# Optimization experiments

Measured on AMD Instinct MI355X. Metric: run time of the kernel, lower is better.

## Reference

```python
import jax, jax.numpy as jnp
import numpy as np

WINDOW = 512
GLOBAL = 64
NEG = -1e9


def setup_inputs() -> dict:
    key = jax.random.key(0)
    kq, kk, kv = jax.random.split(key, 3)
    B, H, S, D = 2, 16, 4096, 64
    q = jax.random.normal(kq, (B, H, S, D), dtype=jnp.float32)
    k = jax.random.normal(kk, (B, H, S, D), dtype=jnp.float32)
    v = jax.random.normal(kv, (B, H, S, D), dtype=jnp.float32)
    return {"q": q, "k": k, "v": v}


def _swa(q, k, v):
    # Causal sliding-window attention (window WINDOW, inclusive of self)
    # with the first GLOBAL queries attending to ALL keys (non-causal),
    # matching the torch reference's per-position SDPA loop.
    B, H, S, D = q.shape
    W, G = WINDOW, GLOBAL
    nb = S // W  # seq chosen as multiple of window
    scale = jnp.asarray(1.0 / np.sqrt(D), q.dtype)

    # --- banded (sliding-window) part, computed blockwise ---
    qb = q.reshape(B, H, nb, W, D)
    # pad one window of zeros in front so each query block sees blocks [b-1, b]
    kp = jnp.pad(k, ((0, 0), (0, 0), (W, 0), (0, 0))).reshape(B, H, nb + 1, W, D)
    vp = jnp.pad(v, ((0, 0), (0, 0), (W, 0), (0, 0))).reshape(B, H, nb + 1, W, D)
    kc = jnp.concatenate([kp[:, :, :nb], kp[:, :, 1:]], axis=3)  # (B,H,nb,2W,D)
    vc = jnp.concatenate([vp[:, :, :nb], vp[:, :, 1:]], axis=3)  # (B,H,nb,2W,D)

    scores = jnp.einsum("bhnqd,bhnkd->bhnqk", qb, kc) * scale  # (B,H,nb,W,2W)

    # query global pos i = b*W + r; key global pos j = (b-1)*W + c, c in [0,2W)
    # window constraint i-W+1 <= j <= i  <=>  r+1 <= c <= r+W
    r = jnp.arange(W)[:, None]
    c = jnp.arange(2 * W)[None, :]
    band = (c >= r + 1) & (c <= r + W)              # (W, 2W)
    first = band & (c >= W)                          # block 0: j >= 0
    blk0 = (jnp.arange(nb) == 0)[:, None, None]
    mask = jnp.where(blk0, first[None], band[None])  # (nb, W, 2W)

    scores = jnp.where(mask[None, None], scores, jnp.asarray(NEG, scores.dtype))
    probs = jax.nn.softmax(scores, axis=-1)
    out = jnp.einsum("bhnqk,bhnkd->bhnqd", probs, vc).reshape(B, H, S, D)

    # --- global prefix: first G queries attend to all keys ---
    sg = jnp.einsum("bhqd,bhkd->bhqk", q[:, :, :G], k) * scale  # (B,H,G,S)
    og = jnp.einsum("bhqk,bhkd->bhqd", jax.nn.softmax(sg, axis=-1), v)
    return out.at[:, :, :G].set(og)


def reference(q, k, v):
    return _swa(q, k, v)
```

## Files before the change

kernel.cpp:

```cpp
#include <hip/hip_runtime.h>


typedef __attribute__((ext_vector_type(4))) float  f32x4;
typedef __attribute__((ext_vector_type(8))) short  s16x8;

#define S_LEN  4096
#define D_HEAD 64
#define SCALE_L2 (0.125f * 1.44269504088896340736f)
#define MINIT  (-1e5f)
#define MASKV  (-1e30f)

static __device__ __forceinline__ short f2bf(float x) {
  unsigned u = __builtin_bit_cast(unsigned, x);
  return (short)((u + 0x8000u) >> 16);
}

static __device__ __forceinline__ f32x4 mfma32(s16x8 a, s16x8 b, f32x4 c) {
  return __builtin_amdgcn_mfma_f32_16x16x32_bf16(a, b, c, 0, 0, 0);
}

struct Stage {
  f32x4 ka[2][2];
  float vs[2][8];
};

static __device__ __forceinline__ void stage_load(const float* __restrict__ K,
                                                  const float* __restrict__ V,
                                                  int k0, int tid, Stage& st) {
#pragma unroll
  for (int i = 0; i < 2; ++i) {
    int s = tid + i * 256;
    int fb = s >> 6, ln = s & 63;
    {
      int row = k0 + ((fb >> 1) << 4) + (ln & 15);
      int d0  = ((fb & 1) << 5) + ((ln >> 4) << 3);
      const float* p = K + row * 64 + d0;
      st.ka[i][0] = *(const f32x4*)p;
      st.ka[i][1] = *(const f32x4*)(p + 4);
    }
    {
      int t = fb >> 2, dt = fb & 3;
      int dd = dt * 16 + (ln & 15);
      int kk = k0 + t * 32 + ((ln >> 4) << 2);
      const float* p = V + kk * 64 + dd;
#pragma unroll
      for (int j = 0; j < 4; ++j) { st.vs[i][j] = p[j * 64]; st.vs[i][4 + j] = p[(16 + j) * 64]; }
    }
  }
}

static __device__ __forceinline__ void stage_write(short* kf, short* vf, int tid, const Stage& st) {
#pragma unroll
  for (int i = 0; i < 2; ++i) {
    int s = tid + i * 256;
    s16x8 kr, vr;
#pragma unroll
    for (int e = 0; e < 4; ++e) { kr[e] = f2bf(st.ka[i][0][e]); kr[4 + e] = f2bf(st.ka[i][1][e]); }
#pragma unroll
    for (int e = 0; e < 8; ++e) vr[e] = f2bf(st.vs[i][e]);
    *(s16x8*)(kf + s * 8) = kr;
    *(s16x8*)(vf + s * 8) = vr;
  }
}

extern "C" __global__ void __launch_bounds__(256, 2)
swa_fused_kernel(const float* __restrict__ qg, const float* __restrict__ kg,
                 const float* __restrict__ vg, float* __restrict__ outg) {
  __shared__ __align__(16) short KB[2][4096];
  __shared__ __align__(16) short VB[2][4096];

  const int tid = threadIdx.x;
  const int w  = tid >> 6;
  const int l  = tid & 63;
  const int g  = l >> 4;
  const int ql = l & 15;
  const int bx = blockIdx.x;
  const int t  = bx >> 5;
  const int bh = bx & 31;

  const float* Q = qg + (size_t)bh * S_LEN * D_HEAD;
  const float* K = kg + (size_t)bh * S_LEN * D_HEAD;
  const float* V = vg + (size_t)bh * S_LEN * D_HEAD;
  float* O = outg + (size_t)bh * S_LEN * D_HEAD;

  Stage st;

  if (t == 0) {
    const int qrow = w * 16 + ql;
    s16x8 qf[2];
#pragma unroll
    for (int h = 0; h < 2; ++h) {
      const float* p = Q + qrow * 64 + h * 32 + g * 8;
      f32x4 a = *(const f32x4*)p, b = *(const f32x4*)(p + 4);
      s16x8 r;
#pragma unroll
      for (int e = 0; e < 4; ++e) { r[e] = f2bf(a[e] * SCALE_L2); r[4 + e] = f2bf(b[e] * SCALE_L2); }
      qf[h] = r;
    }
    f32x4 acc[4] = {{0,0,0,0},{0,0,0,0},{0,0,0,0},{0,0,0,0}};
    float m = MINIT, lsum = 0.f;

    stage_load(K, V, 0, tid, st);
    stage_write(KB[0], VB[0], tid, st);
    __syncthreads();
    int cur = 0;
    for (int kb = 0; kb < 64; ++kb) {
      if (kb < 63) stage_load(K, V, (kb + 1) * 64, tid, st);
      const short* kf = KB[cur];
      const short* vf = VB[cur];
      f32x4 c[4];
#pragma unroll
      for (int kt = 0; kt < 4; ++kt) {
        s16x8 a0 = *(const s16x8*)(kf + ((kt * 2 + 0) * 64 + l) * 8);
        s16x8 a1 = *(const s16x8*)(kf + ((kt * 2 + 1) * 64 + l) * 8);
        f32x4 z = {0,0,0,0};
        z = mfma32(a0, qf[0], z);
        c[kt] = mfma32(a1, qf[1], z);
      }
      float rm = MASKV;
#pragma unroll
      for (int kt = 0; kt < 4; ++kt)
#pragma unroll
        for (int r = 0; r < 4; ++r) rm = fmaxf(rm, c[kt][r]);
      rm = fmaxf(rm, __shfl_xor(rm, 16));
      rm = fmaxf(rm, __shfl_xor(rm, 32));
      float mn = fmaxf(m, rm);
      float al = __builtin_amdgcn_exp2f(m - mn);
      float pv[4][4];
      float rs = 0.f;
#pragma unroll
      for (int kt = 0; kt < 4; ++kt)
#pragma unroll
        for (int r = 0; r < 4; ++r) { float e2 = __builtin_amdgcn_exp2f(c[kt][r] - mn); pv[kt][r] = e2; rs += e2; }
      rs += __shfl_xor(rs, 16);
      rs += __shfl_xor(rs, 32);
      lsum = lsum * al + rs;
      m = mn;
#pragma unroll
      for (int dt = 0; dt < 4; ++dt) acc[dt] *= al;
#pragma unroll
      for (int tt = 0; tt < 2; ++tt) {
        s16x8 pb;
#pragma unroll
        for (int r = 0; r < 4; ++r) { pb[r] = f2bf(pv[2 * tt][r]); pb[4 + r] = f2bf(pv[2 * tt + 1][r]); }
#pragma unroll
        for (int dt = 0; dt < 4; ++dt) {
          s16x8 vfr = *(const s16x8*)(vf + ((tt * 4 + dt) * 64 + l) * 8);
          acc[dt] = mfma32(vfr, pb, acc[dt]);
        }
      }
      if (kb < 63) stage_write(KB[cur ^ 1], VB[cur ^ 1], tid, st);
      __syncthreads();
      cur ^= 1;
    }
    const float inv = 1.0f / lsum;
#pragma unroll
    for (int dt = 0; dt < 4; ++dt) {
      f32x4 o = acc[dt] * inv;
      *(f32x4*)(O + (size_t)qrow * 64 + dt * 16 + g * 4) = o;
    }
    return;
  }

  const int tb = t - 1;
  const int Q0 = tb * 256;
  const int qbase = Q0 + w * 64;

  s16x8 qf[4][2];
#pragma unroll
  for (int qt = 0; qt < 4; ++qt)
#pragma unroll
    for (int h = 0; h < 2; ++h) {
      const float* p = Q + (qbase + qt * 16 + ql) * 64 + h * 32 + g * 8;
      f32x4 a = *(const f32x4*)p, b = *(const f32x4*)(p + 4);
      s16x8 r;
#pragma unroll
      for (int e = 0; e < 4; ++e) { r[e] = f2bf(a[e] * SCALE_L2); r[4 + e] = f2bf(b[e] * SCALE_L2); }
      qf[qt][h] = r;
    }

  f32x4 acc[4][4];
#pragma unroll
  for (int qt = 0; qt < 4; ++qt)
#pragma unroll
    for (int dt = 0; dt < 4; ++dt) acc[qt][dt] = f32x4{0,0,0,0};
  float mm[4] = {MINIT, MINIT, MINIT, MINIT};
  float ll[4] = {0.f, 0.f, 0.f, 0.f};

  const int kbs = (tb >= 2) ? (4 * tb - 8) : 0;
  const int kbe = 4 * tb + 3;

  stage_load(K, V, kbs * 64, tid, st);
  stage_write(KB[0], VB[0], tid, st);
  __syncthreads();
  int cur = 0;
  for (int kb = kbs; kb <= kbe; ++kb) {
    if (kb < kbe) stage_load(K, V, (kb + 1) * 64, tid, st);
    const short* kf = KB[cur];
    const short* vf = VB[cur];

    f32x4 c[4][4];
#pragma unroll
    for (int kt = 0; kt < 4; ++kt) {
      s16x8 a0 = *(const s16x8*)(kf + ((kt * 2 + 0) * 64 + l) * 8);
      s16x8 a1 = *(const s16x8*)(kf + ((kt * 2 + 1) * 64 + l) * 8);
#pragma unroll
      for (int qt = 0; qt < 4; ++qt) {
        f32x4 z = {0,0,0,0};
        z = mfma32(a0, qf[qt][0], z);
        c[qt][kt] = mfma32(a1, qf[qt][1], z);
      }
    }

    const bool needmask = (kb < 4 * tb - 4) || (kb > 4 * tb - 1);

    s16x8 pbq[4][2];
#pragma unroll
    for (int qt = 0; qt < 4; ++qt) {
      const int qrow = qbase + qt * 16 + ql;
      if (needmask) {
#pragma unroll
        for (int kt = 0; kt < 4; ++kt)
#pragma unroll
          for (int r = 0; r < 4; ++r) {
            int j = kb * 64 + kt * 16 + g * 4 + r;
            bool ok = (j <= qrow) && (j >= qrow - 511);
            c[qt][kt][r] = ok ? c[qt][kt][r] : MASKV;
          }
      }
      float rm = MASKV;
#pragma unroll
      for (int kt = 0; kt < 4; ++kt)
#pragma unroll
        for (int r = 0; r < 4; ++r) rm = fmaxf(rm, c[qt][kt][r]);
      rm = fmaxf(rm, __shfl_xor(rm, 16));
      rm = fmaxf(rm, __shfl_xor(rm, 32));
      float mn = fmaxf(mm[qt], rm);
      float al = __builtin_amdgcn_exp2f(mm[qt] - mn);
      float pv[4][4];
      float rs = 0.f;
#pragma unroll
      for (int kt = 0; kt < 4; ++kt)
#pragma unroll
        for (int r = 0; r < 4; ++r) { float e2 = __builtin_amdgcn_exp2f(c[qt][kt][r] - mn); pv[kt][r] = e2; rs += e2; }
      rs += __shfl_xor(rs, 16);
      rs += __shfl_xor(rs, 32);
      ll[qt] = ll[qt] * al + rs;
      mm[qt] = mn;
#pragma unroll
      for (int dt = 0; dt < 4; ++dt) acc[qt][dt] *= al;
#pragma unroll
      for (int tt = 0; tt < 2; ++tt) {
        s16x8 pb;
#pragma unroll
        for (int r = 0; r < 4; ++r) { pb[r] = f2bf(pv[2 * tt][r]); pb[4 + r] = f2bf(pv[2 * tt + 1][r]); }
        pbq[qt][tt] = pb;
      }
    }

#pragma unroll
    for (int tt = 0; tt < 2; ++tt)
#pragma unroll
      for (int dt = 0; dt < 4; ++dt) {
        s16x8 vfr = *(const s16x8*)(vf + ((tt * 4 + dt) * 64 + l) * 8);
#pragma unroll
        for (int qt = 0; qt < 4; ++qt)
          acc[qt][dt] = mfma32(vfr, pbq[qt][tt], acc[qt][dt]);
      }

    if (kb < kbe) stage_write(KB[cur ^ 1], VB[cur ^ 1], tid, st);
    __syncthreads();
    cur ^= 1;
  }

#pragma unroll
  for (int qt = 0; qt < 4; ++qt) {
    if (qbase + qt * 16 >= 64) {
      const int qrow = qbase + qt * 16 + ql;
      const float inv = 1.0f / ll[qt];
#pragma unroll
      for (int dt = 0; dt < 4; ++dt) {
        f32x4 o = acc[qt][dt] * inv;
        *(f32x4*)(O + (size_t)qrow * 64 + dt * 16 + g * 4) = o;
      }
    }
  }
}

extern "C" void kernel_launch(void* const* d_in, const int* in_sizes, int n_in,
                              void* d_out, int out_size, void* d_ws, size_t ws_size,
                              hipStream_t stream) {
  (void)in_sizes; (void)n_in; (void)d_ws; (void)ws_size; (void)out_size;
  const float* q = (const float*)d_in[0];
  const float* k = (const float*)d_in[1];
  const float* v = (const float*)d_in[2];
  float* o = (float*)d_out;
  dim3 grid(17 * 32), block(256);
  hipLaunchKernelGGL(swa_fused_kernel, grid, block, 0, stream, q, k, v, o);
}
```

Before: 193.4 us.

## Split global-prefix attention over key chunks with a separate merge kernel

The global-query blocks, which previously looped over all 4096 keys in one block per head, are split into 8 key chunks handled by separate blocks. Each chunk writes an unnormalized accumulator plus its running max and sum to workspace, and a second kernel merges the chunks flash-decoding style. This removes the long serial tail block that dominated runtime. The cost is extra workspace traffic, a second launch, and the assumption that the workspace is large enough.

```diff
diff --git a/kernel.cpp b/kernel.cpp
--- a/kernel.cpp
+++ b/kernel.cpp
@@ -9,6 +9,8 @@
 #define SCALE_L2 (0.125f * 1.44269504088896340736f)
 #define MINIT  (-1e5f)
 #define MASKV  (-1e30f)
+#define NCHUNK 8
+#define ACC_WS_FLOATS ((size_t)32 * NCHUNK * 64 * 64)
 
 static __device__ __forceinline__ short f2bf(float x) {
   unsigned u = __builtin_bit_cast(unsigned, x);
@@ -65,7 +67,8 @@
 
 extern "C" __global__ void __launch_bounds__(256, 2)
 swa_fused_kernel(const float* __restrict__ qg, const float* __restrict__ kg,
-                 const float* __restrict__ vg, float* __restrict__ outg) {
+                 const float* __restrict__ vg, float* __restrict__ outg,
+                 float* __restrict__ ws) {
   __shared__ __align__(16) short KB[2][4096];
   __shared__ __align__(16) short VB[2][4096];
 
@@ -85,7 +88,8 @@
 
   Stage st;
 
-  if (t == 0) {
+  if (t >= 16) {
+    const int c = t - 16;
     const int qrow = w * 16 + ql;
     s16x8 qf[2];
 #pragma unroll
@@ -100,28 +104,28 @@
     f32x4 acc[4] = {{0,0,0,0},{0,0,0,0},{0,0,0,0},{0,0,0,0}};
     float m = MINIT, lsum = 0.f;
 
-    stage_load(K, V, 0, tid, st);
+    stage_load(K, V, c * 512, tid, st);
     stage_write(KB[0], VB[0], tid, st);
     __syncthreads();
     int cur = 0;
-    for (int kb = 0; kb < 64; ++kb) {
-      if (kb < 63) stage_load(K, V, (kb + 1) * 64, tid, st);
+    for (int kb = 0; kb < 8; ++kb) {
+      if (kb < 7) stage_load(K, V, c * 512 + (kb + 1) * 64, tid, st);
       const short* kf = KB[cur];
       const short* vf = VB[cur];
-      f32x4 c[4];
+      f32x4 cs[4];
 #pragma unroll
       for (int kt = 0; kt < 4; ++kt) {
         s16x8 a0 = *(const s16x8*)(kf + ((kt * 2 + 0) * 64 + l) * 8);
         s16x8 a1 = *(const s16x8*)(kf + ((kt * 2 + 1) * 64 + l) * 8);
         f32x4 z = {0,0,0,0};
         z = mfma32(a0, qf[0], z);
-        c[kt] = mfma32(a1, qf[1], z);
+        cs[kt] = mfma32(a1, qf[1], z);
       }
       float rm = MASKV;
 #pragma unroll
       for (int kt = 0; kt < 4; ++kt)
 #pragma unroll
-        for (int r = 0; r < 4; ++r) rm = fmaxf(rm, c[kt][r]);
+        for (int r = 0; r < 4; ++r) rm = fmaxf(rm, cs[kt][r]);
       rm = fmaxf(rm, __shfl_xor(rm, 16));
       rm = fmaxf(rm, __shfl_xor(rm, 32));
       float mn = fmaxf(m, rm);
@@ -131,7 +135,7 @@
 #pragma unroll
       for (int kt = 0; kt < 4; ++kt)
 #pragma unroll
-        for (int r = 0; r < 4; ++r) { float e2 = __builtin_amdgcn_exp2f(c[kt][r] - mn); pv[kt][r] = e2; rs += e2; }
+        for (int r = 0; r < 4; ++r) { float e2 = __builtin_amdgcn_exp2f(cs[kt][r] - mn); pv[kt][r] = e2; rs += e2; }
       rs += __shfl_xor(rs, 16);
       rs += __shfl_xor(rs, 32);
       lsum = lsum * al + rs;
@@ -149,22 +153,23 @@
           acc[dt] = mfma32(vfr, pb, acc[dt]);
         }
       }
-      if (kb < 63) stage_write(KB[cur ^ 1], VB[cur ^ 1], tid, st);
+      if (kb < 7) stage_write(KB[cur ^ 1], VB[cur ^ 1], tid, st);
       __syncthreads();
       cur ^= 1;
     }
-    const float inv = 1.0f / lsum;
-#pragma unroll
-    for (int dt = 0; dt < 4; ++dt) {
-      f32x4 o = acc[dt] * inv;
-      *(f32x4*)(O + (size_t)qrow * 64 + dt * 16 + g * 4) = o;
+    float* wacc = ws + (((size_t)(bh * NCHUNK + c) * 64) + qrow) * 64;
+#pragma unroll
+    for (int dt = 0; dt < 4; ++dt)
+      *(f32x4*)(wacc + dt * 16 + g * 4) = acc[dt];
+    if (g == 0) {
+      float* wml = ws + ACC_WS_FLOATS + ((size_t)(bh * NCHUNK + c) * 64 + qrow) * 2;
+      wml[0] = m; wml[1] = lsum;
     }
     return;
   }
 
-  const int tb = t - 1;
-  const int Q0 = tb * 256;
-  const int qbase = Q0 + w * 64;
+  const int tb = t;
+  const int qbase = tb * 256 + w * 64;
 
   s16x8 qf[4][2];
 #pragma unroll
@@ -287,14 +292,52 @@
   }
 }
 
+extern "C" __global__ void __launch_bounds__(256)
+swa_merge_kernel(const float* __restrict__ ws, float* __restrict__ outg) {
+  const int bh  = blockIdx.x;
+  const int tid = threadIdx.x;
+  const int row = tid >> 2;
+  const int d0  = (tid & 3) * 16;
+
+  const float* wml = ws + ACC_WS_FLOATS;
+  float mc[NCHUNK], lc[NCHUNK];
+  float M = MASKV;
+#pragma unroll
+  for (int c = 0; c < NCHUNK; ++c) {
+    const float* p = wml + ((size_t)(bh * NCHUNK + c) * 64 + row) * 2;
+    mc[c] = p[0]; lc[c] = p[1];
+    M = fmaxf(M, mc[c]);
+  }
+  float L = 0.f, sc[NCHUNK];
+#pragma unroll
+  for (int c = 0; c < NCHUNK; ++c) { sc[c] = __builtin_amdgcn_exp2f(mc[c] - M); L += lc[c] * sc[c]; }
+  const float inv = 1.0f / L;
+
+  f32x4 o[4] = {{0,0,0,0},{0,0,0,0},{0,0,0,0},{0,0,0,0}};
+#pragma unroll
+  for (int c = 0; c < NCHUNK; ++c) {
+    const float* pa = ws + (((size_t)(bh * NCHUNK + c) * 64) + row) * 64 + d0;
+#pragma unroll
+    for (int j = 0; j < 4; ++j) {
+      f32x4 a = *(const f32x4*)(pa + j * 4);
+      o[j] += a * sc[c];
+    }
+  }
+  float* po = outg + ((size_t)bh * S_LEN + row) * 64 + d0;
+#pragma unroll
+  for (int j = 0; j < 4; ++j) *(f32x4*)(po + j * 4) = o[j] * inv;
+}
+
 extern "C" void kernel_launch(void* const* d_in, const int* in_sizes, int n_in,
                               void* d_out, int out_size, void* d_ws, size_t ws_size,
                               hipStream_t stream) {
-  (void)in_sizes; (void)n_in; (void)d_ws; (void)ws_size; (void)out_size;
+  (void)in_sizes; (void)n_in; (void)ws_size; (void)out_size;
   const float* q = (const float*)d_in[0];
   const float* k = (const float*)d_in[1];
   const float* v = (const float*)d_in[2];
   float* o = (float*)d_out;
-  dim3 grid(17 * 32), block(256);
-  hipLaunchKernelGGL(swa_fused_kernel, grid, block, 0, stream, q, k, v, o);
-}
+  float* ws = (float*)d_ws;
+  dim3 grid(24 * 32), block(256);
+  hipLaunchKernelGGL(swa_fused_kernel, grid, block, 0, stream, q, k, v, o, ws);
+  hipLaunchKernelGGL(swa_merge_kernel, dim3(32), block, 0, stream, ws, o);
+}
```

After: 180.5 us. -6.7%, faster.
